# Kernel tuning notes

Hardware: AMD Instinct MI355X
Metric: run time of the kernel (lower is better)

The kernel has to match this reference:

```python
import jax, jax.numpy as jnp
import numpy as np

BS = 16
CIN = 32          # input_channels
COUT = 64         # out_channels
OUT_DIM = 1024    # out_dim
S = 2
S0 = 1
K = S * (S0 + 1)  # non-overlapping patch size = 4
D = OUT_DIM * K   # input spatial length = 4096


def setup_inputs() -> dict:
    key = jax.random.key(0)
    k1, k2 = jax.random.split(key)
    x = jax.random.normal(k1, (BS, CIN, D), dtype=jnp.float32)
    # learned parameter, torch.randn init
    weight = jax.random.normal(k2, (COUT, CIN, D), dtype=jnp.float32)
    return {"x": x, "weight": weight}


def reference(x, weight):
    # sharing == 0 path of NonOverlappingLocallyConnected1d:
    #   out[b,o,p] = (1/sqrt(CIN)) * sum_{c,k} x[b,c,p*K+k] * weight[o,c,p*K+k]
    # Original materializes [bs,cout,cin,D] via broadcast multiply then sums
    # over (cin, K); fused here as a single einsum over non-overlapping patches.
    bs = x.shape[0]
    xr = x.reshape(bs, CIN, OUT_DIM, K)        # [b, c, p, k]
    wr = weight.reshape(COUT, CIN, OUT_DIM, K)  # [o, c, p, k]
    out = jnp.einsum('bcpk,ocpk->bop', xr, wr)  # [b, o, p]
    return out / jnp.sqrt(jnp.asarray(CIN, x.dtype))
```

## Files before the change

kernel.cpp:

```cpp
#include <hip/hip_runtime.h>

#define BS      16
#define CIN     32
#define COUT    64
#define OUT_DIM 1024
#define RS4     1024

#define OT      8
#define PT      32

__global__ __launch_bounds__(1024, 4) void nolc1d_kernel(
    const float* __restrict__ x,
    const float* __restrict__ w,
    float* __restrict__ out)
{
    const int bid = blockIdx.x;
    const int xcd = bid & 7;
    const int r   = bid >> 3;
    const int og  = r & 7;
    const int pg  = xcd + 8 * (r >> 3);
    const int o0  = og * OT;
    const int pf0 = pg * PT;

    const int t    = threadIdx.x;
    const int lane = t & 63;
    const int wv   = t >> 6;
    const int g    = wv & 3;
    const int csh  = wv >> 2;
    const int cs   = (csh << 1) | (lane >> 5);
    const int pp   = lane & 31;

    __shared__ float4 red[4096];

    const float4* __restrict__ x4 = (const float4*)x;
    const float4* __restrict__ w4 = (const float4*)w;

    float acc[4][OT] = {};
    const int xb = ((4 * g) * CIN + cs) * RS4 + pf0 + pp;
    const int wb = (o0 * CIN + cs) * RS4 + pf0 + pp;

    #pragma unroll 2
    for (int j = 0; j < 4; ++j) {
        float4 xv[4];
        #pragma unroll
        for (int bi = 0; bi < 4; ++bi)
            xv[bi] = x4[xb + bi * (CIN * RS4) + j * (8 * RS4)];
        #pragma unroll
        for (int o = 0; o < OT; ++o) {
            const float4 wq = w4[wb + o * (CIN * RS4) + j * (8 * RS4)];
            #pragma unroll
            for (int bi = 0; bi < 4; ++bi)
                acc[bi][o] += xv[bi].x * wq.x + xv[bi].y * wq.y +
                              xv[bi].z * wq.z + xv[bi].w * wq.w;
        }
    }

    #pragma unroll
    for (int bi = 0; bi < 4; ++bi)
        #pragma unroll
        for (int o = 0; o < OT; ++o)
            acc[bi][o] += __shfl_xor(acc[bi][o], 32, 64);

    if (lane < 32) {
        #pragma unroll
        for (int o = 0; o < OT; ++o)
            red[((csh * 4 + g) * 8 + o) * 32 + pp] =
                make_float4(acc[0][o], acc[1][o], acc[2][o], acc[3][o]);
    }
    __syncthreads();

    const float scale = 0.17677669529663687f;
    const int idx = t;
    const int g2  = idx >> 8;
    const int oo  = (idx >> 5) & 7;
    const int p2  = idx & 31;
    const float4 a = red[idx];
    const float4 b = red[idx + 1024];
    const float4 c = red[idx + 2048];
    const float4 d = red[idx + 3072];
    const int p = pf0 + p2;
    out[((4 * g2 + 0) * COUT + o0 + oo) * OUT_DIM + p] =
        (a.x + b.x + c.x + d.x) * scale;
    out[((4 * g2 + 1) * COUT + o0 + oo) * OUT_DIM + p] =
        (a.y + b.y + c.y + d.y) * scale;
    out[((4 * g2 + 2) * COUT + o0 + oo) * OUT_DIM + p] =
        (a.z + b.z + c.z + d.z) * scale;
    out[((4 * g2 + 3) * COUT + o0 + oo) * OUT_DIM + p] =
        (a.w + b.w + c.w + d.w) * scale;
}

extern "C" void kernel_launch(void* const* d_in, const int* in_sizes, int n_in,
                              void* d_out, int out_size, void* d_ws, size_t ws_size,
                              hipStream_t stream) {
    const float* x = (const float*)d_in[0];
    const float* w = (const float*)d_in[1];
    float* out = (float*)d_out;

    nolc1d_kernel<<<dim3(256), dim3(1024), 0, stream>>>(x, w, out);
}
```

Before: 87.52 us.

## Split work into smaller 4x4 batch-output tiles over many 256-thread blocks

Each block now covers 4 batches, 4 output channels and 32 patches, using 256 threads instead of 1024. The grid grows from 256 to 2048 blocks, giving more independent blocks per CU and a smaller shared-memory reduction. The cost is reuse: weight tiles are reloaded once per batch group and input tiles once per output group, so cache and memory traffic rise. The channel loop is also no longer unrolled, which reduces instruction-level parallelism.

```diff
diff --git a/kernel.cpp b/kernel.cpp
--- a/kernel.cpp
+++ b/kernel.cpp
@@ -6,48 +6,42 @@
 #define OUT_DIM 1024
 #define RS4     1024
 
-#define OT      8
-#define PT      32
-
-__global__ __launch_bounds__(1024, 4) void nolc1d_kernel(
+__global__ __launch_bounds__(256, 6) void nolc1d_kernel(
     const float* __restrict__ x,
     const float* __restrict__ w,
     float* __restrict__ out)
 {
     const int bid = blockIdx.x;
     const int xcd = bid & 7;
-    const int r   = bid >> 3;
-    const int og  = r & 7;
-    const int pg  = xcd + 8 * (r >> 3);
-    const int o0  = og * OT;
-    const int pf0 = pg * PT;
+    const int j   = bid >> 3;
+    const int og  = j & 15;
+    const int bs  = (j >> 4) & 3;
+    const int pg  = xcd + 8 * (j >> 6);
+    const int o0  = og * 4;
+    const int b0  = bs * 4;
+    const int pf0 = pg * 32;
 
     const int t    = threadIdx.x;
     const int lane = t & 63;
     const int wv   = t >> 6;
-    const int g    = wv & 3;
-    const int csh  = wv >> 2;
-    const int cs   = (csh << 1) | (lane >> 5);
-    const int pp   = lane & 31;
-
-    __shared__ float4 red[4096];
+    const int cs   = t >> 5;
+    const int pp   = t & 31;
 
     const float4* __restrict__ x4 = (const float4*)x;
     const float4* __restrict__ w4 = (const float4*)w;
 
-    float acc[4][OT] = {};
-    const int xb = ((4 * g) * CIN + cs) * RS4 + pf0 + pp;
-    const int wb = (o0 * CIN + cs) * RS4 + pf0 + pp;
+    float acc[4][4] = {};
 
-    #pragma unroll 2
-    for (int j = 0; j < 4; ++j) {
+    #pragma unroll 1
+    for (int k = 0; k < 4; ++k) {
+        const int c = cs + 8 * k;
         float4 xv[4];
         #pragma unroll
         for (int bi = 0; bi < 4; ++bi)
-            xv[bi] = x4[xb + bi * (CIN * RS4) + j * (8 * RS4)];
+            xv[bi] = x4[((b0 + bi) * CIN + c) * RS4 + pf0 + pp];
         #pragma unroll
-        for (int o = 0; o < OT; ++o) {
-            const float4 wq = w4[wb + o * (CIN * RS4) + j * (8 * RS4)];
+        for (int o = 0; o < 4; ++o) {
+            const float4 wq = w4[((o0 + o) * CIN + c) * RS4 + pf0 + pp];
             #pragma unroll
             for (int bi = 0; bi < 4; ++bi)
                 acc[bi][o] += xv[bi].x * wq.x + xv[bi].y * wq.y +
@@ -58,35 +52,31 @@
     #pragma unroll
     for (int bi = 0; bi < 4; ++bi)
         #pragma unroll
-        for (int o = 0; o < OT; ++o)
+        for (int o = 0; o < 4; ++o)
             acc[bi][o] += __shfl_xor(acc[bi][o], 32, 64);
 
+    __shared__ float red[4][4][4][32];
     if (lane < 32) {
         #pragma unroll
-        for (int o = 0; o < OT; ++o)
-            red[((csh * 4 + g) * 8 + o) * 32 + pp] =
-                make_float4(acc[0][o], acc[1][o], acc[2][o], acc[3][o]);
+        for (int bi = 0; bi < 4; ++bi)
+            #pragma unroll
+            for (int o = 0; o < 4; ++o)
+                red[wv][bi][o][pp] = acc[bi][o];
     }
     __syncthreads();
 
     const float scale = 0.17677669529663687f;
-    const int idx = t;
-    const int g2  = idx >> 8;
-    const int oo  = (idx >> 5) & 7;
-    const int p2  = idx & 31;
-    const float4 a = red[idx];
-    const float4 b = red[idx + 1024];
-    const float4 c = red[idx + 2048];
-    const float4 d = red[idx + 3072];
-    const int p = pf0 + p2;
-    out[((4 * g2 + 0) * COUT + o0 + oo) * OUT_DIM + p] =
-        (a.x + b.x + c.x + d.x) * scale;
-    out[((4 * g2 + 1) * COUT + o0 + oo) * OUT_DIM + p] =
-        (a.y + b.y + c.y + d.y) * scale;
-    out[((4 * g2 + 2) * COUT + o0 + oo) * OUT_DIM + p] =
-        (a.z + b.z + c.z + d.z) * scale;
-    out[((4 * g2 + 3) * COUT + o0 + oo) * OUT_DIM + p] =
-        (a.w + b.w + c.w + d.w) * scale;
+    #pragma unroll
+    for (int rep = 0; rep < 2; ++rep) {
+        const int idx = t + 256 * rep;
+        const int b   = idx >> 7;
+        const int o   = (idx >> 5) & 3;
+        const int p2  = idx & 31;
+        const float s = red[0][b][o][p2] + red[1][b][o][p2] +
+                        red[2][b][o][p2] + red[3][b][o][p2];
+        out[((size_t)(b0 + b) * COUT + o0 + o) * OUT_DIM + pg * 32 + p2] =
+            s * scale;
+    }
 }
 
 extern "C" void kernel_launch(void* const* d_in, const int* in_sizes, int n_in,
@@ -96,5 +86,5 @@
     const float* w = (const float*)d_in[1];
     float* out = (float*)d_out;
 
-    nolc1d_kernel<<<dim3(256), dim3(1024), 0, stream>>>(x, w, out);
+    nolc1d_kernel<<<dim3(2048), dim3(256), 0, stream>>>(x, w, out);
 }
```

New measurement: 87.12 us. Within noise of the previous version (-0.5%).
